# Optimization experiments

Hardware: AMD Instinct MI355X
Metric: run time of the kernel (lower is better)

## Reference

```python
import jax, jax.numpy as jnp
import numpy as np

B, S, K, N = 4, 2048, 4096, 11008
GROUP_SIZE = 128
NUM_GROUPS = K // GROUP_SIZE  # 32


def setup_inputs() -> dict:
    key = jax.random.key(0)
    k1, k2, k3, k4, k5 = jax.random.split(key, 5)
    x = jax.random.normal(k1, (B, S, K), dtype=jnp.float32)
    # sensitivity-sorted column order is a permutation of [0, K)
    col_indices = jax.random.permutation(k2, K).astype(jnp.int32)
    # packed uint8 nibbles stored as int32 in [0, 256)
    w_packed = jax.random.randint(k3, (K // 2, N), 0, 256, dtype=jnp.int32)
    # per-group, per-output-column dequant scales (positive, small)
    scales = (jax.random.uniform(k4, (NUM_GROUPS, N), dtype=jnp.float32) + 0.05) * 0.01
    bias = jax.random.normal(k5, (N,), dtype=jnp.float32) * 0.01
    return {"x": x, "col_indices": col_indices, "w_packed": w_packed,
            "scales": scales, "bias": bias}


def _dequant_weight(w_packed, scales):
    # unpack int4 nibbles: low nibble -> even k, high nibble -> odd k
    low = (w_packed & 15) - 8          # [K//2, N]
    high = ((w_packed >> 4) & 15) - 8  # [K//2, N]
    w_int = jnp.stack([low, high], axis=1).reshape(K, N)  # interleaved [K, N]
    # per-group dequant: scale index = k // group_size
    w = w_int.astype(scales.dtype).reshape(NUM_GROUPS, GROUP_SIZE, N)
    w = w * scales[:, None, :]
    return w.reshape(K, N)


def reference(x, col_indices, w_packed, scales, bias):
    orig_shape = x.shape
    xm = x.reshape(-1, K)                     # [M, K]
    xg = jnp.take(xm, col_indices, axis=1)    # column-reorder gather [M, K]
    w = _dequant_weight(w_packed, scales)     # [K, N]
    out = jnp.einsum('mk,kn->mn', xg, w)      # fp32 accumulate
    out = out + bias
    return out.reshape(orig_shape[0], orig_shape[1], N)
```

## Files before the change

kernel.cpp:

```cpp
#include <hip/hip_runtime.h>
#include <hip/hip_bf16.h>
#include <stdint.h>

#define M_DIM 8192
#define K_DIM 4096
#define N_DIM 11008

typedef __attribute__((ext_vector_type(8))) short bf16x8;
typedef __attribute__((ext_vector_type(4))) float f32x4;
typedef __attribute__((ext_vector_type(4))) unsigned int uint4v;

__device__ __forceinline__ unsigned short f2bf(float f) {
    __hip_bfloat16 h = __float2bfloat16(f);
    return __builtin_bit_cast(unsigned short, h);
}

__device__ __forceinline__ void gload_lds16(const unsigned short* g, unsigned short* l) {
    __builtin_amdgcn_global_load_lds(
        (const __attribute__((address_space(1))) void*)g,
        (__attribute__((address_space(3))) void*)l,
        16, 0, 0);
}

__device__ __forceinline__ unsigned lds_addr(const unsigned short* p) {
    return (unsigned)(uintptr_t)(const __attribute__((address_space(3))) unsigned short*)p;
}

#define DSRI(dst, a, OFF) asm volatile("ds_read_b128 %0, %1 offset:%2" \
    : "=v"(dst) : "v"(a), "n"(OFF) : "memory")

#define LGKM(N) do { \
    asm volatile("s_waitcnt lgkmcnt(" #N ")" ::: "memory"); \
    __builtin_amdgcn_sched_barrier(0); \
} while (0)
#define VMC(N) asm volatile("s_waitcnt vmcnt(" #N ")" ::: "memory")
#define BAR() do { __builtin_amdgcn_s_barrier(); asm volatile("" ::: "memory"); } while (0)

__global__ void permute_x_kernel(const float* __restrict__ x,
                                 const int* __restrict__ ci,
                                 unsigned short* __restrict__ xg) {
    int idx = blockIdx.x * 256 + threadIdx.x;
    int64_t base = (int64_t)idx * 4;
    int m = (int)(base >> 12);
    int k = (int)(base & 4095);
    const float* xrow = x + ((int64_t)m << 12);
    int4 c4 = *reinterpret_cast<const int4*>(ci + k);
    ushort4 o;
    o.x = f2bf(xrow[c4.x]);
    o.y = f2bf(xrow[c4.y]);
    o.z = f2bf(xrow[c4.z]);
    o.w = f2bf(xrow[c4.w]);
    *reinterpret_cast<ushort4*>(xg + base) = o;
}

__global__ void dequant_w_kernel(const int* __restrict__ wp,
                                 const float* __restrict__ scales,
                                 unsigned short* __restrict__ wT) {
    __shared__ unsigned short tile[64][65];
    int n0 = blockIdx.x * 64;
    int k0 = blockIdx.y * 64;
    int g = k0 >> 7;
    int t = threadIdx.x;
    int col = t & 63;
    int r0 = t >> 6;
    float s = scales[(int64_t)g * N_DIM + n0 + col];
    int pr0 = k0 >> 1;
#pragma unroll
    for (int i = 0; i < 8; ++i) {
        int row = r0 + i * 4;
        int p = wp[(int64_t)(pr0 + row) * N_DIM + n0 + col];
        tile[2 * row][col]     = f2bf((float)((p & 15) - 8) * s);
        tile[2 * row + 1][col] = f2bf((float)(((p >> 4) & 15) - 8) * s);
    }
    __syncthreads();
    int nl = t >> 2;
    int kk0 = (t & 3) << 4;
    unsigned short vals[16];
#pragma unroll
    for (int j = 0; j < 16; ++j) vals[j] = tile[kk0 + j][nl];
    uint4v* dst = reinterpret_cast<uint4v*>(wT + (int64_t)(n0 + nl) * K_DIM + k0 + kk0);
    dst[0] = *reinterpret_cast<const uint4v*>(&vals[0]);
    dst[1] = *reinterpret_cast<const uint4v*>(&vals[8]);
}


template <int BUF>
__device__ __forceinline__ void read_RA(bf16x8 (&a)[4], bf16x8 (&b)[4],
                                        unsigned aA01, unsigned aA23,
                                        unsigned bB01, unsigned bB23) {
    const unsigned ad = (BUF < 2) ? aA01 : aA23;
    const unsigned bd = (BUF < 2) ? bB01 : bB23;
    constexpr int bo = (BUF & 1) * 32768;
    DSRI(a[0], ad, bo + 0);
    DSRI(a[1], ad, bo + 1024);
    DSRI(a[2], ad, bo + 2048);
    DSRI(a[3], ad, bo + 3072);
    DSRI(b[0], bd, bo + 0);
    DSRI(b[1], bd, bo + 1024);
    DSRI(b[2], bd, bo + 2048);
    DSRI(b[3], bd, bo + 3072);
}

template <int BUF>
__device__ __forceinline__ void read_RB(bf16x8 (&a2)[4], unsigned aA01, unsigned aA23) {
    const unsigned ad = (BUF < 2) ? aA01 : aA23;
    constexpr int bo = (BUF & 1) * 32768;
    DSRI(a2[0], ad, bo + 4096);
    DSRI(a2[1], ad, bo + 5120);
    DSRI(a2[2], ad, bo + 6144);
    DSRI(a2[3], ad, bo + 7168);
}

template <int MB>
__device__ __forceinline__ void mfma4(f32x4 (&acc)[8][4], const bf16x8 (&av)[4],
                                      const bf16x8 (&bv)[4]) {
#pragma unroll
    for (int m = 0; m < 4; ++m)
#pragma unroll
        for (int n = 0; n < 4; ++n)
            acc[MB + m][n] = __builtin_amdgcn_mfma_f32_16x16x32_bf16(
                av[m], bv[n], acc[MB + m][n], 0, 0, 0);
}

template <int DBUF, int ISB>
__device__ __forceinline__ void stage2(const unsigned short* p0, const unsigned short* p1,
                                       int t, unsigned short* lds, int wLds) {
    const unsigned short* s0 = p0 + t * 32;
    const unsigned short* s1 = p1 + t * 32;
    unsigned short* d = lds + DBUF * 16384 + ISB * 8192 + wLds;
    gload_lds16(s0, d);
    gload_lds16(s1, d + 512);
}

#define PH_TILE(B, BN, BS, CA_, CB_, NA_, NB_, tt)                        \
    do {                                                                  \
        read_RB<B>(a2, aA01, aA23);                                       \
        stage2<BS, 0>(pA0, pA1, (tt), lds, wLds);                         \
        LGKM(4);                                                          \
        mfma4<0>(acc, CA_, CB_);                                          \
        VMC(6);                                                           \
        BAR();                                                            \
        read_RA<BN>(NA_, NB_, aA01, aA23, bB01, bB23);                    \
        stage2<BS, 1>(pB0, pB1, (tt), lds, wLds);                         \
        LGKM(8);                                                          \
        mfma4<4>(acc, a2, CB_);                                           \
        BAR();                                                            \
    } while (0)

__global__ __launch_bounds__(512, 2)
void gemm_kernel(const unsigned short* __restrict__ A,
                 const unsigned short* __restrict__ BT,
                 const float* __restrict__ bias,
                 float* __restrict__ C) {
    __shared__ unsigned short lds[65536];

    constexpr int NT = N_DIM / 256;
    int wg = blockIdx.x, nwg = gridDim.x;
    int q = nwg >> 3, r = nwg & 7;
    int xcd = wg & 7, li = wg >> 3;
    int swz = (xcd < r ? xcd * (q + 1) : r * (q + 1) + (xcd - r) * q) + li;
    int by = swz / NT, bx = swz - by * NT;
    int brow = by << 8, bcol = bx << 8;

    int t = threadIdx.x;
    int lane = t & 63, w = t >> 6;
    int wr = w >> 2, wc = w & 3;
    int fr = lane & 15, fq = lane >> 4;

    const unsigned xr = (unsigned)((fr & 6) << 3);
    const int riw = lane >> 2;
    const int s8 = ((lane & 3) ^ ((lane >> 3) & 3)) << 3;
    const int w32 = w * 32, wLds = w * 1024;

    const unsigned ldsB = lds_addr(lds);
    const unsigned aA01 = ldsB + ((unsigned)((wr * 128 + fr) * 64 + fq * 16) ^ xr);
    const unsigned bB01 = ldsB + 16384u + ((unsigned)((wc * 64 + fr) * 64 + fq * 16) ^ xr);
    const unsigned aA23 = aA01 + 65536;
    const unsigned bB23 = bB01 + 65536;

    const unsigned short* pA0 = A + (int64_t)(brow + w32 + riw) * K_DIM + s8;
    const unsigned short* pA1 = pA0 + 16 * K_DIM;
    const unsigned short* pB0 = BT + (int64_t)(bcol + w32 + riw) * K_DIM + s8;
    const unsigned short* pB1 = pB0 + 16 * K_DIM;

    f32x4 acc[8][4];
#pragma unroll
    for (int m = 0; m < 8; ++m)
#pragma unroll
        for (int n = 0; n < 4; ++n) acc[m][n] = (f32x4){0.f, 0.f, 0.f, 0.f};

    bf16x8 aX[4], bX[4], aY[4], bY[4], a2[4];

    stage2<0, 0>(pA0, pA1, 0, lds, wLds);
    stage2<0, 1>(pB0, pB1, 0, lds, wLds);
    stage2<1, 0>(pA0, pA1, 1, lds, wLds);
    stage2<1, 1>(pB0, pB1, 1, lds, wLds);
    stage2<2, 0>(pA0, pA1, 2, lds, wLds);
    stage2<2, 1>(pB0, pB1, 2, lds, wLds);
    VMC(8);
    BAR();
    read_RA<0>(aX, bX, aA01, aA23, bB01, bB23);

#pragma unroll 1
    for (int body = 0; body < 31; ++body) {
        const int t3 = body * 4 + 3;
        PH_TILE(0, 1, 3, aX, bX, aY, bY, t3);
        PH_TILE(1, 2, 0, aY, bY, aX, bX, t3 + 1);
        PH_TILE(2, 3, 1, aX, bX, aY, bY, t3 + 2);
        PH_TILE(3, 0, 2, aY, bY, aX, bX, t3 + 3);
    }

    PH_TILE(0, 1, 3, aX, bX, aY, bY, 127);
    read_RB<1>(a2, aA01, aA23);
    LGKM(4);
    mfma4<0>(acc, aY, bY);
    VMC(4);
    BAR();
    read_RA<2>(aX, bX, aA01, aA23, bB01, bB23);
    LGKM(8);
    mfma4<4>(acc, a2, bY);
    BAR();
    read_RB<2>(a2, aA01, aA23);
    LGKM(4);
    mfma4<0>(acc, aX, bX);
    VMC(0);
    BAR();
    read_RA<3>(aY, bY, aA01, aA23, bB01, bB23);
    LGKM(8);
    mfma4<4>(acc, a2, bX);
    BAR();
    read_RB<3>(a2, aA01, aA23);
    LGKM(4);
    mfma4<0>(acc, aY, bY);
    LGKM(0);
    mfma4<4>(acc, a2, bY);

    int orow0 = brow + wr * 128 + fq * 4;
    int ocol0 = bcol + wc * 64 + fr;
#pragma unroll
    for (int n = 0; n < 4; ++n) {
        int col = ocol0 + n * 16;
        float bval = bias[col];
#pragma unroll
        for (int m = 0; m < 8; ++m) {
            int row = orow0 + m * 16;
            float* cp = C + (int64_t)row * N_DIM + col;
#pragma unroll
            for (int j = 0; j < 4; ++j) {
                cp[(int64_t)j * N_DIM] = acc[m][n][j] + bval;
            }
        }
    }
}

extern "C" void kernel_launch(void* const* d_in, const int* in_sizes, int n_in,
                              void* d_out, int out_size, void* d_ws, size_t ws_size,
                              hipStream_t stream) {
    const float* x      = (const float*)d_in[0];
    const int* ci       = (const int*)d_in[1];
    const int* wp       = (const int*)d_in[2];
    const float* scales = (const float*)d_in[3];
    const float* bias   = (const float*)d_in[4];
    float* out          = (float*)d_out;

    const size_t wT_bytes = (size_t)N_DIM * K_DIM * 2;
    unsigned short* wT = (unsigned short*)d_ws;
    unsigned short* xg = wT + (size_t)N_DIM * K_DIM;

    size_t cap = (ws_size > wT_bytes) ? (ws_size - wT_bytes) : 0;
    int max_rows = (int)(cap / ((size_t)K_DIM * 2));
    int chunk_rows = (max_rows / 256) * 256;
    if (chunk_rows <= 0) chunk_rows = 256;
    if (chunk_rows > M_DIM) chunk_rows = M_DIM;

    dequant_w_kernel<<<dim3(N_DIM / 64, K_DIM / 64), 256, 0, stream>>>(wp, scales, wT);

    for (int m0 = 0; m0 < M_DIM; m0 += chunk_rows) {
        int rows = M_DIM - m0 < chunk_rows ? M_DIM - m0 : chunk_rows;
        int pgrid = (int)(((int64_t)rows * K_DIM) / (4 * 256));
        permute_x_kernel<<<pgrid, 256, 0, stream>>>(
            x + (int64_t)m0 * K_DIM, ci, xg);
        int grid = (rows / 256) * (N_DIM / 256);
        gemm_kernel<<<grid, 512, 0, stream>>>(
            xg, wT, bias, out + (int64_t)m0 * N_DIM);
    }
}
```

Measured before the change: 813.7 us.

## Split B-fragment LDS reads across phases to rebalance MFMA/LDS overlap

Restructures the per-tile LDS read schedule. The B operand fragments are now split into two halves, with the second half loaded alongside the A rows 4-7, and the MFMA work is issued in four 4x2 quadrants instead of two 4x4 halves. This lets the second-phase MFMAs run with no LDS wait after the barrier, and it trims register pressure for the B fragments. The cost is an extra LGKM wait inside the first phase, and the loads are ordered differently relative to the barriers.

```diff
diff --git a/kernel.cpp b/kernel.cpp
--- a/kernel.cpp
+++ b/kernel.cpp
@@ -85,41 +85,44 @@
 
 
 template <int BUF>
-__device__ __forceinline__ void read_RA(bf16x8 (&a)[4], bf16x8 (&b)[4],
+__device__ __forceinline__ void read_R1(bf16x8 (&a03)[4], bf16x8 (&b01)[2],
                                         unsigned aA01, unsigned aA23,
                                         unsigned bB01, unsigned bB23) {
     const unsigned ad = (BUF < 2) ? aA01 : aA23;
     const unsigned bd = (BUF < 2) ? bB01 : bB23;
     constexpr int bo = (BUF & 1) * 32768;
-    DSRI(a[0], ad, bo + 0);
-    DSRI(a[1], ad, bo + 1024);
-    DSRI(a[2], ad, bo + 2048);
-    DSRI(a[3], ad, bo + 3072);
-    DSRI(b[0], bd, bo + 0);
-    DSRI(b[1], bd, bo + 1024);
-    DSRI(b[2], bd, bo + 2048);
-    DSRI(b[3], bd, bo + 3072);
+    DSRI(a03[0], ad, bo + 0);
+    DSRI(a03[1], ad, bo + 1024);
+    DSRI(a03[2], ad, bo + 2048);
+    DSRI(a03[3], ad, bo + 3072);
+    DSRI(b01[0], bd, bo + 0);
+    DSRI(b01[1], bd, bo + 1024);
 }
 
 template <int BUF>
-__device__ __forceinline__ void read_RB(bf16x8 (&a2)[4], unsigned aA01, unsigned aA23) {
+__device__ __forceinline__ void read_R2(bf16x8 (&a47)[4], bf16x8 (&b23)[2],
+                                        unsigned aA01, unsigned aA23,
+                                        unsigned bB01, unsigned bB23) {
     const unsigned ad = (BUF < 2) ? aA01 : aA23;
+    const unsigned bd = (BUF < 2) ? bB01 : bB23;
     constexpr int bo = (BUF & 1) * 32768;
-    DSRI(a2[0], ad, bo + 4096);
-    DSRI(a2[1], ad, bo + 5120);
-    DSRI(a2[2], ad, bo + 6144);
-    DSRI(a2[3], ad, bo + 7168);
-}
-
-template <int MB>
-__device__ __forceinline__ void mfma4(f32x4 (&acc)[8][4], const bf16x8 (&av)[4],
-                                      const bf16x8 (&bv)[4]) {
+    DSRI(a47[0], ad, bo + 4096);
+    DSRI(a47[1], ad, bo + 5120);
+    DSRI(a47[2], ad, bo + 6144);
+    DSRI(a47[3], ad, bo + 7168);
+    DSRI(b23[0], bd, bo + 2048);
+    DSRI(b23[1], bd, bo + 3072);
+}
+
+template <int MB, int NB>
+__device__ __forceinline__ void mfma8(f32x4 (&acc)[8][4], const bf16x8 (&av)[4],
+                                      const bf16x8 (&bv)[2]) {
 #pragma unroll
     for (int m = 0; m < 4; ++m)
 #pragma unroll
-        for (int n = 0; n < 4; ++n)
-            acc[MB + m][n] = __builtin_amdgcn_mfma_f32_16x16x32_bf16(
-                av[m], bv[n], acc[MB + m][n], 0, 0, 0);
+        for (int n = 0; n < 2; ++n)
+            acc[MB + m][NB + n] = __builtin_amdgcn_mfma_f32_16x16x32_bf16(
+                av[m], bv[n], acc[MB + m][NB + n], 0, 0, 0);
 }
 
 template <int DBUF, int ISB>
@@ -132,18 +135,20 @@
     gload_lds16(s1, d + 512);
 }
 
-#define PH_TILE(B, BN, BS, CA_, CB_, NA_, NB_, tt)                        \
+#define PH_TILE(B, BN, BS, A1_, B1_, NA1_, NB1_, tt)                      \
     do {                                                                  \
-        read_RB<B>(a2, aA01, aA23);                                       \
+        read_R2<B>(a2, b2, aA01, aA23, bB01, bB23);                       \
         stage2<BS, 0>(pA0, pA1, (tt), lds, wLds);                         \
-        LGKM(4);                                                          \
-        mfma4<0>(acc, CA_, CB_);                                          \
+        LGKM(6);                                                          \
+        mfma8<0, 0>(acc, A1_, B1_);                                       \
+        LGKM(0);                                                          \
+        mfma8<4, 0>(acc, a2, B1_);                                        \
         VMC(6);                                                           \
         BAR();                                                            \
-        read_RA<BN>(NA_, NB_, aA01, aA23, bB01, bB23);                    \
+        read_R1<BN>(NA1_, NB1_, aA01, aA23, bB01, bB23);                  \
         stage2<BS, 1>(pB0, pB1, (tt), lds, wLds);                         \
-        LGKM(8);                                                          \
-        mfma4<4>(acc, a2, CB_);                                           \
+        mfma8<0, 2>(acc, A1_, b2);                                        \
+        mfma8<4, 2>(acc, a2, b2);                                         \
         BAR();                                                            \
     } while (0)
 
@@ -189,7 +194,7 @@
 #pragma unroll
         for (int n = 0; n < 4; ++n) acc[m][n] = (f32x4){0.f, 0.f, 0.f, 0.f};
 
-    bf16x8 aX[4], bX[4], aY[4], bY[4], a2[4];
+    bf16x8 aX[4], bX[2], aY[4], bY[2], a2[4], b2[2];
 
     stage2<0, 0>(pA0, pA1, 0, lds, wLds);
     stage2<0, 1>(pB0, pB1, 0, lds, wLds);
@@ -199,7 +204,7 @@
     stage2<2, 1>(pB0, pB1, 2, lds, wLds);
     VMC(8);
     BAR();
-    read_RA<0>(aX, bX, aA01, aA23, bB01, bB23);
+    read_R1<0>(aX, bX, aA01, aA23, bB01, bB23);
 
 #pragma unroll 1
     for (int body = 0; body < 31; ++body) {
@@ -211,29 +216,35 @@
     }
 
     PH_TILE(0, 1, 3, aX, bX, aY, bY, 127);
-    read_RB<1>(a2, aA01, aA23);
-    LGKM(4);
-    mfma4<0>(acc, aY, bY);
+    read_R2<1>(a2, b2, aA01, aA23, bB01, bB23);
+    LGKM(6);
+    mfma8<0, 0>(acc, aY, bY);
+    LGKM(0);
+    mfma8<4, 0>(acc, a2, bY);
     VMC(4);
     BAR();
-    read_RA<2>(aX, bX, aA01, aA23, bB01, bB23);
-    LGKM(8);
-    mfma4<4>(acc, a2, bY);
-    BAR();
-    read_RB<2>(a2, aA01, aA23);
-    LGKM(4);
-    mfma4<0>(acc, aX, bX);
+    read_R1<2>(aX, bX, aA01, aA23, bB01, bB23);
+    mfma8<0, 2>(acc, aY, b2);
+    mfma8<4, 2>(acc, a2, b2);
+    BAR();
+    read_R2<2>(a2, b2, aA01, aA23, bB01, bB23);
+    LGKM(6);
+    mfma8<0, 0>(acc, aX, bX);
+    LGKM(0);
+    mfma8<4, 0>(acc, a2, bX);
     VMC(0);
     BAR();
-    read_RA<3>(aY, bY, aA01, aA23, bB01, bB23);
-    LGKM(8);
-    mfma4<4>(acc, a2, bX);
-    BAR();
-    read_RB<3>(a2, aA01, aA23);
-    LGKM(4);
-    mfma4<0>(acc, aY, bY);
+    read_R1<3>(aY, bY, aA01, aA23, bB01, bB23);
+    mfma8<0, 2>(acc, aX, b2);
+    mfma8<4, 2>(acc, a2, b2);
+    BAR();
+    read_R2<3>(a2, b2, aA01, aA23, bB01, bB23);
+    LGKM(6);
+    mfma8<0, 0>(acc, aY, bY);
     LGKM(0);
-    mfma4<4>(acc, a2, bY);
+    mfma8<4, 0>(acc, a2, bY);
+    mfma8<0, 2>(acc, aY, b2);
+    mfma8<4, 2>(acc, a2, b2);
 
     int orow0 = brow + wr * 128 + fq * 4;
     int ocol0 = bcol + wc * 64 + fr;
```

Result: no change. 809.2 us (-0.6%).
